# Kernel tuning notes

Measured on AMD Instinct MI355X. Metric: run time of the kernel, lower is better.

## Reference

```python
import jax, jax.numpy as jnp
import numpy as np

TAU = 1.0
EPS = 1e-6
M_FEATURES = 256
HEAD_DIM = 64


def _make_projection(m, d, seed=0):
    # FAVOR+ projection: stacked transposed-Q blocks from QR of Gaussian blocks,
    # rows rescaled by norms of iid Gaussian rows (scaling=0 in the torch code).
    rng = np.random.RandomState(seed)
    blocks = []
    for _ in range(m // d):
        q, _ = np.linalg.qr(rng.randn(d, d))
        blocks.append(q.T)
    rem = m - (m // d) * d
    if rem > 0:
        q, _ = np.linalg.qr(rng.randn(d, d))
        blocks.append(q.T[:rem])
    mat = np.vstack(blocks)
    multiplier = np.linalg.norm(rng.randn(m, d), axis=1)
    return jnp.asarray(multiplier[:, None] * mat, dtype=jnp.float32)


def setup_inputs() -> dict:
    key = jax.random.key(0)
    k1, k2, k3 = jax.random.split(key, 3)
    b, n, h, d = 4, 4096, 8, HEAD_DIM
    return {
        "x": jax.random.normal(k1, (b, n, h, d), dtype=jnp.float32),
        "node_vec1": jax.random.normal(k2, (b, n, h, d), dtype=jnp.float32),
        "node_vec2": jax.random.normal(k3, (b, n, h, d), dtype=jnp.float32),
        "projection_matrix": _make_projection(M_FEATURES, d, seed=0),
    }


def _random_feature_map(data, is_query, projection_matrix):
    d = data.shape[-1]
    data = data * (float(d) ** -0.25)  # data_normalizer = 1/sqrt(sqrt(d))
    ratio = float(projection_matrix.shape[0]) ** -0.5
    data_dash = jnp.einsum('bnhd,md->bnhm', data, projection_matrix)
    diag_data = jnp.sum(data * data, axis=-1, keepdims=True) * 0.5  # [b,n,h,1]
    if is_query:
        stab = jnp.max(data_dash, axis=-1, keepdims=True)  # per-position max
    else:
        # max over feature dim then over node dim (axis 1)
        stab = jnp.max(jnp.max(data_dash, axis=-1, keepdims=True), axis=1, keepdims=True)
    return ratio * (jnp.exp(data_dash - diag_data - stab) + EPS)


def reference(x, node_vec1, node_vec2, projection_matrix):
    inv_sqrt_tau = 1.0 / np.sqrt(TAU)
    v1p = _random_feature_map(node_vec1 * inv_sqrt_tau, True, projection_matrix)
    v2p = _random_feature_map(node_vec2 * inv_sqrt_tau, False, projection_matrix)
    # Linear (kernelized) attention via associativity: O(n*m*d) not O(n^2)
    v2x = jnp.einsum('bnhm,bnhd->bhmd', v2p, x)
    out1 = jnp.einsum('bnhm,bhmd->bnhd', v1p, v2x)
    v2_sum = jnp.sum(v2p, axis=1)  # [b,h,m]
    out2 = jnp.einsum('bnhm,bhm->bnh', v1p, v2_sum)
    return (out1 / out2[..., None], v1p, v2p)
```

## Files before the change

kernel.cpp:

```cpp
#include <hip/hip_runtime.h>
#include <math.h>


namespace {
constexpr int B_ = 4, N_ = 4096, H_ = 8, D_ = 64, M_ = 256;
constexpr int BH_ = B_ * H_;
constexpr int POS_ = B_ * N_ * H_;
constexpr float SCALE_ = 0.35355339059327378f;
constexpr float RATIO_ = 0.0625f;
constexpr float FEPS_ = 1e-6f;

constexpr int WS_BHMAX = 0;
constexpr int WS_V2X   = 32;
constexpr int WS_V2SUM = WS_V2X + BH_ * M_ * D_;
constexpr int WS_DIAG1 = WS_V2SUM + BH_ * M_;
constexpr int WS_DIAG2 = WS_DIAG1 + POS_;
constexpr int WS_ZERO_END = WS_DIAG1;
}

__device__ __forceinline__ void atomicMaxF(float* addr, float v) {
  if (v >= 0.f)
    atomicMax((int*)addr, __float_as_int(v));
  else
    atomicMin((unsigned int*)addr, __float_as_uint(v));
}

__global__ void k_init(float* __restrict__ ws) {
  int i = blockIdx.x * 256 + threadIdx.x;
  int stride = gridDim.x * 256;
  for (; i < WS_ZERO_END; i += stride) {
    ws[i] = (i < 32) ? -INFINITY : 0.f;
  }
}

__global__ void k_diag(const float* __restrict__ v1, const float* __restrict__ v2,
                       float* __restrict__ ws) {
  int t = threadIdx.x;
  int r = t >> 2, seg = t & 3;
  int rowg = blockIdx.x * 64 + r;
  const float* src;
  float* dst;
  int row;
  if (rowg < POS_) { src = v1; dst = ws + WS_DIAG1; row = rowg; }
  else             { src = v2; dst = ws + WS_DIAG2; row = rowg - POS_; }
  const float4* p = reinterpret_cast<const float4*>(src + (size_t)row * 64) + seg * 4;
  float s = 0.f;
#pragma unroll
  for (int j = 0; j < 4; ++j) {
    float4 v = p[j];
    s = fmaf(v.x, v.x, s); s = fmaf(v.y, v.y, s);
    s = fmaf(v.z, v.z, s); s = fmaf(v.w, v.w, s);
  }
  s += __shfl_xor(s, 1);
  s += __shfl_xor(s, 2);
  if (seg == 0) dst[row] = 0.0625f * s;
}

template <bool IS_QUERY>
__global__ __launch_bounds__(256) void k_proj(const float* __restrict__ vec,
                                              const float* __restrict__ Pm,
                                              float* __restrict__ ddout,
                                              float* __restrict__ ws) {
  int t = threadIdx.x;
  int bh = blockIdx.x >> 5;
  int tile = blockIdx.x & 31;
  int b = bh >> 3, h = bh & 7;

  float4 pr[16];
  {
    const float4* pp = reinterpret_cast<const float4*>(Pm + t * 64);
#pragma unroll
    for (int j = 0; j < 16; ++j) {
      float4 v = pp[j];
      pr[j].x = v.x * SCALE_; pr[j].y = v.y * SCALE_;
      pr[j].z = v.z * SCALE_; pr[j].w = v.w * SCALE_;
    }
  }

  __shared__ float wmax[2][4][8];
  __shared__ float wm[4];
  int wv = t >> 6, ln = t & 63;
  float vmax = -INFINITY;
  const float* diag1 = ws + WS_DIAG1;

  int nbase = tile * 128;
  for (int chunk = 0; chunk < 16; ++chunk) {
    float a[8];
#pragma unroll
    for (int cp = 0; cp < 8; ++cp) {
      int n = nbase + chunk * 8 + cp;
      int pg = (b * N_ + n) * H_ + h;
      const float4* r4 = reinterpret_cast<const float4*>(vec + (size_t)pg * 64);
      float acc = 0.f;
#pragma unroll
      for (int j = 0; j < 16; ++j) {
        float4 dv = r4[j];
        acc = fmaf(dv.x, pr[j].x, acc);
        acc = fmaf(dv.y, pr[j].y, acc);
        acc = fmaf(dv.z, pr[j].z, acc);
        acc = fmaf(dv.w, pr[j].w, acc);
      }
      a[cp] = acc;
    }
    if (IS_QUERY) {
      int buf = chunk & 1;
#pragma unroll
      for (int cp = 0; cp < 8; ++cp) {
        float m = a[cp];
#pragma unroll
        for (int o = 1; o < 64; o <<= 1) m = fmaxf(m, __shfl_xor(m, o));
        if (ln == 0) wmax[buf][wv][cp] = m;
      }
      __syncthreads();
#pragma unroll
      for (int cp = 0; cp < 8; ++cp) {
        int n = nbase + chunk * 8 + cp;
        int pg = (b * N_ + n) * H_ + h;
        float mx = fmaxf(fmaxf(wmax[buf][0][cp], wmax[buf][1][cp]),
                         fmaxf(wmax[buf][2][cp], wmax[buf][3][cp]));
        float dgv = diag1[pg];
        float val = RATIO_ * (__expf(a[cp] - dgv - mx) + FEPS_);
        ddout[pg * M_ + t] = val;
      }
    } else {
#pragma unroll
      for (int cp = 0; cp < 8; ++cp) {
        vmax = fmaxf(vmax, a[cp]);
        int n = nbase + chunk * 8 + cp;
        int pg = (b * N_ + n) * H_ + h;
        ddout[pg * M_ + t] = a[cp];
      }
    }
  }
  if (!IS_QUERY) {
#pragma unroll
    for (int o = 1; o < 64; o <<= 1) vmax = fmaxf(vmax, __shfl_xor(vmax, o));
    if (ln == 0) wm[wv] = vmax;
    __syncthreads();
    if (t == 0) {
      float m = fmaxf(fmaxf(wm[0], wm[1]), fmaxf(wm[2], wm[3]));
      atomicMaxF(ws + WS_BHMAX + bh, m);
    }
  }
}

__global__ __launch_bounds__(256) void k_v2accum(const float* __restrict__ x,
                                                 float* __restrict__ v2p,
                                                 float* __restrict__ ws) {
  __shared__ float sP[32][264];
  __shared__ float sX[32][64];
  int t = threadIdx.x;
  int bh = blockIdx.x >> 4, chunk = blockIdx.x & 15;
  int b = bh >> 3, h = bh & 7;
  int n0 = chunk * 256;
  float bhmax = ws[WS_BHMAX + bh];
  const float* diag2 = ws + WS_DIAG2;

  int mg = t & 31, dgi = t >> 5;
  int pl8 = t >> 3, seg = t & 7;

  float acc[8][8];
  float acc2[8];
#pragma unroll
  for (int i = 0; i < 8; ++i) {
    acc2[i] = 0.f;
#pragma unroll
    for (int j = 0; j < 8; ++j) acc[i][j] = 0.f;
  }

  for (int it = 0; it < 8; ++it) {
    __syncthreads();
    {
      int n = n0 + it * 32 + pl8;
      int pg = (b * N_ + n) * H_ + h;
      float dgv = diag2[pg];
      float* gp = v2p + (size_t)pg * M_;
#pragma unroll
      for (int j = 0; j < 8; ++j) {
        int m = seg * 4 + j * 32;
        float4 dv = *reinterpret_cast<const float4*>(gp + m);
        float4 vv;
        vv.x = RATIO_ * (__expf(dv.x - dgv - bhmax) + FEPS_);
        vv.y = RATIO_ * (__expf(dv.y - dgv - bhmax) + FEPS_);
        vv.z = RATIO_ * (__expf(dv.z - dgv - bhmax) + FEPS_);
        vv.w = RATIO_ * (__expf(dv.w - dgv - bhmax) + FEPS_);
        *reinterpret_cast<float4*>(gp + m) = vv;
        *reinterpret_cast<float4*>(&sP[pl8][m]) = vv;
      }
      const float* gx = x + (size_t)pg * 64;
#pragma unroll
      for (int j = 0; j < 2; ++j) {
        int f = seg * 2 + j;
        float4 xv = *reinterpret_cast<const float4*>(gx + f * 4);
        *reinterpret_cast<float4*>(&sX[pl8][f * 4]) = xv;
      }
    }
    __syncthreads();
#pragma unroll 4
    for (int nn = 0; nn < 32; ++nn) {
      float4 a0 = *reinterpret_cast<const float4*>(&sP[nn][mg * 8]);
      float4 a1 = *reinterpret_cast<const float4*>(&sP[nn][mg * 8 + 4]);
      float4 b0 = *reinterpret_cast<const float4*>(&sX[nn][dgi * 8]);
      float4 b1 = *reinterpret_cast<const float4*>(&sX[nn][dgi * 8 + 4]);
      float av[8] = {a0.x, a0.y, a0.z, a0.w, a1.x, a1.y, a1.z, a1.w};
      float bv[8] = {b0.x, b0.y, b0.z, b0.w, b1.x, b1.y, b1.z, b1.w};
#pragma unroll
      for (int i = 0; i < 8; ++i) {
        acc2[i] += av[i];
#pragma unroll
        for (int j = 0; j < 8; ++j) acc[i][j] = fmaf(av[i], bv[j], acc[i][j]);
      }
    }
  }

  float* vx = ws + WS_V2X + bh * M_ * D_;
#pragma unroll
  for (int i = 0; i < 8; ++i)
#pragma unroll
    for (int j = 0; j < 8; ++j)
      atomicAdd(vx + (mg * 8 + i) * 64 + dgi * 8 + j, acc[i][j]);
  if (dgi == 0) {
    float* vs = ws + WS_V2SUM + bh * M_;
#pragma unroll
    for (int i = 0; i < 8; ++i) atomicAdd(vs + mg * 8 + i, acc2[i]);
  }
}

__global__ __launch_bounds__(256) void k_pv(const float* __restrict__ v1p,
                                            float* __restrict__ ws,
                                            float* __restrict__ out) {
  __shared__ float sA[64][129];
  __shared__ float sB[128][68];
  __shared__ float sVs[256];
  int t = threadIdx.x;
  int bh = blockIdx.x >> 6, tile = blockIdx.x & 63;
  int b = bh >> 3, h = bh & 7;
  int n0 = tile * 64;
  int pg_ = t & 15, dg = t >> 4;
  int pl = t >> 2, sseg = t & 3;
  int mr = t >> 1, hseg = t & 1;

  if (t < 64) {
    float4 v = *reinterpret_cast<const float4*>(ws + WS_V2SUM + bh * M_ + t * 4);
    *reinterpret_cast<float4*>(&sVs[t * 4]) = v;
  }

  float acc1[4][4];
  float acc2[4];
#pragma unroll
  for (int i = 0; i < 4; ++i) {
    acc2[i] = 0.f;
#pragma unroll
    for (int j = 0; j < 4; ++j) acc1[i][j] = 0.f;
  }

  int posg_base = (b * N_ + n0) * H_ + h;

  for (int half = 0; half < 2; ++half) {
    __syncthreads();
    int m0 = half * 128;
    {
      int pg = posg_base + pl * H_;
      const float* gp = v1p + (size_t)pg * M_ + m0;
#pragma unroll
      for (int j = 0; j < 8; ++j) {
        int m = sseg * 4 + j * 16;
        float4 v = *reinterpret_cast<const float4*>(gp + m);
        sA[pl][m] = v.x; sA[pl][m + 1] = v.y;
        sA[pl][m + 2] = v.z; sA[pl][m + 3] = v.w;
      }
      const float* gb = ws + WS_V2X + bh * M_ * D_ + (m0 + mr) * 64 + hseg * 32;
#pragma unroll
      for (int j = 0; j < 8; ++j) {
        float4 v = *reinterpret_cast<const float4*>(gb + j * 4);
        *reinterpret_cast<float4*>(&sB[mr][hseg * 32 + j * 4]) = v;
      }
    }
    __syncthreads();
#pragma unroll 4
    for (int m = 0; m < 128; ++m) {
      float a0 = sA[4 * pg_ + 0][m];
      float a1 = sA[4 * pg_ + 1][m];
      float a2 = sA[4 * pg_ + 2][m];
      float a3 = sA[4 * pg_ + 3][m];
      float4 bv = *reinterpret_cast<const float4*>(&sB[m][dg * 4]);
      float vsm = sVs[m0 + m];
      acc1[0][0] = fmaf(a0, bv.x, acc1[0][0]); acc1[0][1] = fmaf(a0, bv.y, acc1[0][1]);
      acc1[0][2] = fmaf(a0, bv.z, acc1[0][2]); acc1[0][3] = fmaf(a0, bv.w, acc1[0][3]);
      acc1[1][0] = fmaf(a1, bv.x, acc1[1][0]); acc1[1][1] = fmaf(a1, bv.y, acc1[1][1]);
      acc1[1][2] = fmaf(a1, bv.z, acc1[1][2]); acc1[1][3] = fmaf(a1, bv.w, acc1[1][3]);
      acc1[2][0] = fmaf(a2, bv.x, acc1[2][0]); acc1[2][1] = fmaf(a2, bv.y, acc1[2][1]);
      acc1[2][2] = fmaf(a2, bv.z, acc1[2][2]); acc1[2][3] = fmaf(a2, bv.w, acc1[2][3]);
      acc1[3][0] = fmaf(a3, bv.x, acc1[3][0]); acc1[3][1] = fmaf(a3, bv.y, acc1[3][1]);
      acc1[3][2] = fmaf(a3, bv.z, acc1[3][2]); acc1[3][3] = fmaf(a3, bv.w, acc1[3][3]);
      acc2[0] = fmaf(a0, vsm, acc2[0]);
      acc2[1] = fmaf(a1, vsm, acc2[1]);
      acc2[2] = fmaf(a2, vsm, acc2[2]);
      acc2[3] = fmaf(a3, vsm, acc2[3]);
    }
  }

#pragma unroll
  for (int i = 0; i < 4; ++i) {
    int pg = posg_base + (4 * pg_ + i) * H_;
    float inv = 1.f / acc2[i];
    float4 o;
    o.x = acc1[i][0] * inv; o.y = acc1[i][1] * inv;
    o.z = acc1[i][2] * inv; o.w = acc1[i][3] * inv;
    *reinterpret_cast<float4*>(out + (size_t)pg * 64 + dg * 4) = o;
  }
}

extern "C" void kernel_launch(void* const* d_in, const int* in_sizes, int n_in,
                              void* d_out, int out_size, void* d_ws, size_t ws_size,
                              hipStream_t stream) {
  const float* x  = (const float*)d_in[0];
  const float* v1 = (const float*)d_in[1];
  const float* v2 = (const float*)d_in[2];
  const float* Pm = (const float*)d_in[3];
  float* out = (float*)d_out;
  float* v1p = out + (size_t)POS_ * D_;
  float* v2p = v1p + (size_t)POS_ * M_;
  float* ws = (float*)d_ws;

  k_init<<<1024, 256, 0, stream>>>(ws);
  k_diag<<<2 * POS_ / 64, 256, 0, stream>>>(v1, v2, ws);
  k_proj<false><<<BH_ * 32, 256, 0, stream>>>(v2, Pm, v2p, ws);
  k_proj<true><<<BH_ * 32, 256, 0, stream>>>(v1, Pm, v1p, ws);
  k_v2accum<<<BH_ * 16, 256, 0, stream>>>(x, v2p, ws);
  k_pv<<<BH_ * 64, 256, 0, stream>>>(v1p, ws, out);
}
```

Before: 1.015 ms.

## Stage projection inputs in LDS, split v2 accumulation by feature quarter, add deterministic partial reduce

k_proj now loads its 128-row input tile into shared memory once instead of re-reading it from global memory per thread, and the key path stores exp(dash - diag) directly. k_v2accum then only needs to rescale by a per-bh factor exp(-max) with a single FMA rather than a full exp. k_v2accum is split four ways across the feature dimension, giving 2048 blocks with smaller per-thread accumulators for more parallelism and lower register pressure. When the workspace is large enough, partial results go to a buffer and a new reduce kernel sums them instead of issuing atomics. k_pv uses 64-wide m-phases with smaller shared tiles. Factoring exp(-max) out of the stored exp changes rounding slightly and could overflow if the raw logits are large.

```diff
diff --git a/kernel.cpp b/kernel.cpp
--- a/kernel.cpp
+++ b/kernel.cpp
@@ -15,6 +15,9 @@
 constexpr int WS_V2SUM = WS_V2X + BH_ * M_ * D_;
 constexpr int WS_DIAG1 = WS_V2SUM + BH_ * M_;
 constexpr int WS_DIAG2 = WS_DIAG1 + POS_;
+constexpr int WS_PART  = WS_DIAG2 + POS_;
+constexpr int WS_PSUM  = WS_PART + 16 * 32 * 4 * 4096;
+constexpr int WS_END   = WS_PSUM + 16 * 32 * 4 * 64;
 constexpr int WS_ZERO_END = WS_DIAG1;
 }
 
@@ -57,13 +60,15 @@
 }
 
 template <bool IS_QUERY>
-__global__ __launch_bounds__(256) void k_proj(const float* __restrict__ vec,
-                                              const float* __restrict__ Pm,
-                                              float* __restrict__ ddout,
-                                              float* __restrict__ ws) {
+__global__ __launch_bounds__(256, 4) void k_proj(const float* __restrict__ vec,
+                                                 const float* __restrict__ Pm,
+                                                 float* __restrict__ ddout,
+                                                 float* __restrict__ ws) {
+  __shared__ float4 sD[128 * 16];
+  __shared__ float wmax[2][4][8];
+  __shared__ float wm[4];
   int t = threadIdx.x;
-  int bh = blockIdx.x >> 5;
-  int tile = blockIdx.x & 31;
+  int bh = blockIdx.x >> 5, tile = blockIdx.x & 31;
   int b = bh >> 3, h = bh & 7;
 
   float4 pr[16];
@@ -77,24 +82,32 @@
     }
   }
 
-  __shared__ float wmax[2][4][8];
-  __shared__ float wm[4];
+  {
+    const float* base = vec + ((size_t)(b * N_ + tile * 128) * H_ + h) * 64;
+    int r0 = t >> 4, fq = t & 15;
+#pragma unroll
+    for (int i = 0; i < 8; ++i) {
+      int row = i * 16 + r0;
+      sD[row * 16 + fq] =
+          *reinterpret_cast<const float4*>(base + (size_t)row * 512 + fq * 4);
+    }
+  }
+  __syncthreads();
+
   int wv = t >> 6, ln = t & 63;
-  float vmax = -INFINITY;
-  const float* diag1 = ws + WS_DIAG1;
-
-  int nbase = tile * 128;
-  for (int chunk = 0; chunk < 16; ++chunk) {
+  const float* diag = ws + (IS_QUERY ? WS_DIAG1 : WS_DIAG2);
+  int pgbase = (b * N_ + tile * 128) * H_ + h;
+  float vmaxk = -INFINITY;
+
+  for (int grp = 0; grp < 16; ++grp) {
     float a[8];
 #pragma unroll
     for (int cp = 0; cp < 8; ++cp) {
-      int n = nbase + chunk * 8 + cp;
-      int pg = (b * N_ + n) * H_ + h;
-      const float4* r4 = reinterpret_cast<const float4*>(vec + (size_t)pg * 64);
+      const float4* rp = &sD[(grp * 8 + cp) * 16];
       float acc = 0.f;
 #pragma unroll
       for (int j = 0; j < 16; ++j) {
-        float4 dv = r4[j];
+        float4 dv = rp[j];
         acc = fmaf(dv.x, pr[j].x, acc);
         acc = fmaf(dv.y, pr[j].y, acc);
         acc = fmaf(dv.z, pr[j].z, acc);
@@ -103,7 +116,7 @@
       a[cp] = acc;
     }
     if (IS_QUERY) {
-      int buf = chunk & 1;
+      int buf = grp & 1;
 #pragma unroll
       for (int cp = 0; cp < 8; ++cp) {
         float m = a[cp];
@@ -114,131 +127,149 @@
       __syncthreads();
 #pragma unroll
       for (int cp = 0; cp < 8; ++cp) {
-        int n = nbase + chunk * 8 + cp;
-        int pg = (b * N_ + n) * H_ + h;
+        int pg = pgbase + (grp * 8 + cp) * H_;
         float mx = fmaxf(fmaxf(wmax[buf][0][cp], wmax[buf][1][cp]),
                          fmaxf(wmax[buf][2][cp], wmax[buf][3][cp]));
-        float dgv = diag1[pg];
-        float val = RATIO_ * (__expf(a[cp] - dgv - mx) + FEPS_);
-        ddout[pg * M_ + t] = val;
+        ddout[(size_t)pg * M_ + t] = RATIO_ * (__expf(a[cp] - diag[pg] - mx) + FEPS_);
       }
     } else {
 #pragma unroll
       for (int cp = 0; cp < 8; ++cp) {
-        vmax = fmaxf(vmax, a[cp]);
-        int n = nbase + chunk * 8 + cp;
-        int pg = (b * N_ + n) * H_ + h;
-        ddout[pg * M_ + t] = a[cp];
+        int pg = pgbase + (grp * 8 + cp) * H_;
+        vmaxk = fmaxf(vmaxk, a[cp]);
+        ddout[(size_t)pg * M_ + t] = __expf(a[cp] - diag[pg]);
       }
     }
   }
   if (!IS_QUERY) {
 #pragma unroll
-    for (int o = 1; o < 64; o <<= 1) vmax = fmaxf(vmax, __shfl_xor(vmax, o));
-    if (ln == 0) wm[wv] = vmax;
-    __syncthreads();
-    if (t == 0) {
-      float m = fmaxf(fmaxf(wm[0], wm[1]), fmaxf(wm[2], wm[3]));
-      atomicMaxF(ws + WS_BHMAX + bh, m);
-    }
+    for (int o = 1; o < 64; o <<= 1) vmaxk = fmaxf(vmaxk, __shfl_xor(vmaxk, o));
+    if (ln == 0) wm[wv] = vmaxk;
+    __syncthreads();
+    if (t == 0)
+      atomicMaxF(ws + WS_BHMAX + bh, fmaxf(fmaxf(wm[0], wm[1]), fmaxf(wm[2], wm[3])));
   }
 }
 
 __global__ __launch_bounds__(256) void k_v2accum(const float* __restrict__ x,
                                                  float* __restrict__ v2p,
-                                                 float* __restrict__ ws) {
-  __shared__ float sP[32][264];
-  __shared__ float sX[32][64];
+                                                 float* __restrict__ ws, int use_part) {
+  __shared__ float sE[16][68];
+  __shared__ float sX[16][68];
   int t = threadIdx.x;
-  int bh = blockIdx.x >> 4, chunk = blockIdx.x & 15;
+  int bx = blockIdx.x;
+  int chunk = bx & 15, mq = (bx >> 4) & 3, bh = bx >> 6;
   int b = bh >> 3, h = bh & 7;
   int n0 = chunk * 256;
-  float bhmax = ws[WS_BHMAX + bh];
-  const float* diag2 = ws + WS_DIAG2;
-
-  int mg = t & 31, dgi = t >> 5;
-  int pl8 = t >> 3, seg = t & 7;
-
-  float acc[8][8];
-  float acc2[8];
-#pragma unroll
-  for (int i = 0; i < 8; ++i) {
-    acc2[i] = 0.f;
+  float rs = RATIO_ * __expf(-ws[WS_BHMAX + bh]);
+  float re = RATIO_ * FEPS_;
+
+  int mg = t >> 3, dgi = t & 7;
+  int r0 = t >> 4, fq = t & 15;
+
+  float acc[2][8];
+  float acc2[2] = {0.f, 0.f};
+#pragma unroll
+  for (int i = 0; i < 2; ++i)
 #pragma unroll
     for (int j = 0; j < 8; ++j) acc[i][j] = 0.f;
-  }
-
-  for (int it = 0; it < 8; ++it) {
+
+  for (int it = 0; it < 16; ++it) {
     __syncthreads();
     {
-      int n = n0 + it * 32 + pl8;
-      int pg = (b * N_ + n) * H_ + h;
-      float dgv = diag2[pg];
-      float* gp = v2p + (size_t)pg * M_;
-#pragma unroll
-      for (int j = 0; j < 8; ++j) {
-        int m = seg * 4 + j * 32;
-        float4 dv = *reinterpret_cast<const float4*>(gp + m);
-        float4 vv;
-        vv.x = RATIO_ * (__expf(dv.x - dgv - bhmax) + FEPS_);
-        vv.y = RATIO_ * (__expf(dv.y - dgv - bhmax) + FEPS_);
-        vv.z = RATIO_ * (__expf(dv.z - dgv - bhmax) + FEPS_);
-        vv.w = RATIO_ * (__expf(dv.w - dgv - bhmax) + FEPS_);
-        *reinterpret_cast<float4*>(gp + m) = vv;
-        *reinterpret_cast<float4*>(&sP[pl8][m]) = vv;
-      }
-      const float* gx = x + (size_t)pg * 64;
-#pragma unroll
-      for (int j = 0; j < 2; ++j) {
-        int f = seg * 2 + j;
-        float4 xv = *reinterpret_cast<const float4*>(gx + f * 4);
-        *reinterpret_cast<float4*>(&sX[pl8][f * 4]) = xv;
-      }
+      size_t pg = (size_t)(b * N_ + n0 + it * 16 + r0) * H_ + h;
+      float* gp = v2p + pg * M_ + mq * 64 + fq * 4;
+      float4 ev = *reinterpret_cast<const float4*>(gp);
+      float4 vv;
+      vv.x = fmaf(ev.x, rs, re); vv.y = fmaf(ev.y, rs, re);
+      vv.z = fmaf(ev.z, rs, re); vv.w = fmaf(ev.w, rs, re);
+      *reinterpret_cast<float4*>(gp) = vv;
+      *reinterpret_cast<float4*>(&sE[r0][fq * 4]) = vv;
+      float4 xv = *reinterpret_cast<const float4*>(x + pg * 64 + fq * 4);
+      *reinterpret_cast<float4*>(&sX[r0][fq * 4]) = xv;
     }
     __syncthreads();
 #pragma unroll 4
-    for (int nn = 0; nn < 32; ++nn) {
-      float4 a0 = *reinterpret_cast<const float4*>(&sP[nn][mg * 8]);
-      float4 a1 = *reinterpret_cast<const float4*>(&sP[nn][mg * 8 + 4]);
+    for (int nn = 0; nn < 16; ++nn) {
+      float2 ev = *reinterpret_cast<const float2*>(&sE[nn][mg * 2]);
       float4 b0 = *reinterpret_cast<const float4*>(&sX[nn][dgi * 8]);
       float4 b1 = *reinterpret_cast<const float4*>(&sX[nn][dgi * 8 + 4]);
-      float av[8] = {a0.x, a0.y, a0.z, a0.w, a1.x, a1.y, a1.z, a1.w};
-      float bv[8] = {b0.x, b0.y, b0.z, b0.w, b1.x, b1.y, b1.z, b1.w};
-#pragma unroll
-      for (int i = 0; i < 8; ++i) {
-        acc2[i] += av[i];
-#pragma unroll
-        for (int j = 0; j < 8; ++j) acc[i][j] = fmaf(av[i], bv[j], acc[i][j]);
-      }
-    }
-  }
-
-  float* vx = ws + WS_V2X + bh * M_ * D_;
-#pragma unroll
-  for (int i = 0; i < 8; ++i)
-#pragma unroll
-    for (int j = 0; j < 8; ++j)
-      atomicAdd(vx + (mg * 8 + i) * 64 + dgi * 8 + j, acc[i][j]);
-  if (dgi == 0) {
-    float* vs = ws + WS_V2SUM + bh * M_;
-#pragma unroll
-    for (int i = 0; i < 8; ++i) atomicAdd(vs + mg * 8 + i, acc2[i]);
+      acc2[0] += ev.x; acc2[1] += ev.y;
+      acc[0][0] = fmaf(ev.x, b0.x, acc[0][0]); acc[0][1] = fmaf(ev.x, b0.y, acc[0][1]);
+      acc[0][2] = fmaf(ev.x, b0.z, acc[0][2]); acc[0][3] = fmaf(ev.x, b0.w, acc[0][3]);
+      acc[0][4] = fmaf(ev.x, b1.x, acc[0][4]); acc[0][5] = fmaf(ev.x, b1.y, acc[0][5]);
+      acc[0][6] = fmaf(ev.x, b1.z, acc[0][6]); acc[0][7] = fmaf(ev.x, b1.w, acc[0][7]);
+      acc[1][0] = fmaf(ev.y, b0.x, acc[1][0]); acc[1][1] = fmaf(ev.y, b0.y, acc[1][1]);
+      acc[1][2] = fmaf(ev.y, b0.z, acc[1][2]); acc[1][3] = fmaf(ev.y, b0.w, acc[1][3]);
+      acc[1][4] = fmaf(ev.y, b1.x, acc[1][4]); acc[1][5] = fmaf(ev.y, b1.y, acc[1][5]);
+      acc[1][6] = fmaf(ev.y, b1.z, acc[1][6]); acc[1][7] = fmaf(ev.y, b1.w, acc[1][7]);
+    }
+  }
+
+  if (use_part) {
+    float* pp = ws + WS_PART + (((size_t)chunk * BH_ + bh) * 4 + mq) * 4096;
+#pragma unroll
+    for (int i = 0; i < 2; ++i) {
+      float* q = pp + (mg * 2 + i) * 64 + dgi * 8;
+      *reinterpret_cast<float4*>(q)     = make_float4(acc[i][0], acc[i][1], acc[i][2], acc[i][3]);
+      *reinterpret_cast<float4*>(q + 4) = make_float4(acc[i][4], acc[i][5], acc[i][6], acc[i][7]);
+    }
+    if (dgi == 0) {
+      float* ps = ws + WS_PSUM + (((size_t)chunk * BH_ + bh) * 4 + mq) * 64 + mg * 2;
+      ps[0] = acc2[0]; ps[1] = acc2[1];
+    }
+  } else {
+    float* vx = ws + WS_V2X + (size_t)bh * M_ * D_;
+#pragma unroll
+    for (int i = 0; i < 2; ++i)
+#pragma unroll
+      for (int j = 0; j < 8; ++j)
+        atomicAdd(vx + (mq * 64 + mg * 2 + i) * 64 + dgi * 8 + j, acc[i][j]);
+    if (dgi == 0) {
+      float* vs = ws + WS_V2SUM + (size_t)bh * M_;
+#pragma unroll
+      for (int i = 0; i < 2; ++i) atomicAdd(vs + mq * 64 + mg * 2 + i, acc2[i]);
+    }
+  }
+}
+
+__global__ void k_reduce(float* __restrict__ ws) {
+  int i = blockIdx.x * 256 + threadIdx.x;
+  if (i < 131072) {
+    int bh = i >> 12, rem = i & 4095;
+    int m = rem >> 4, dq = rem & 15;
+    int mq = m >> 6, mloc = m & 63;
+    float4 s = make_float4(0.f, 0.f, 0.f, 0.f);
+#pragma unroll
+    for (int c = 0; c < 16; ++c) {
+      const float4 v = *reinterpret_cast<const float4*>(
+          ws + WS_PART + (((size_t)c * BH_ + bh) * 4 + mq) * 4096 + mloc * 64 + dq * 4);
+      s.x += v.x; s.y += v.y; s.z += v.z; s.w += v.w;
+    }
+    *reinterpret_cast<float4*>(ws + WS_V2X + (size_t)i * 4) = s;
+  } else if (i < 131072 + 8192) {
+    int j = i - 131072;
+    int bh = j >> 8, m = j & 255;
+    int mq = m >> 6, mloc = m & 63;
+    float s = 0.f;
+#pragma unroll
+    for (int c = 0; c < 16; ++c)
+      s += ws[WS_PSUM + (((size_t)c * BH_ + bh) * 4 + mq) * 64 + mloc];
+    ws[WS_V2SUM + j] = s;
   }
 }
 
 __global__ __launch_bounds__(256) void k_pv(const float* __restrict__ v1p,
                                             float* __restrict__ ws,
                                             float* __restrict__ out) {
-  __shared__ float sA[64][129];
-  __shared__ float sB[128][68];
+  __shared__ float sA[64][67];
+  __shared__ float sB[64][68];
   __shared__ float sVs[256];
   int t = threadIdx.x;
   int bh = blockIdx.x >> 6, tile = blockIdx.x & 63;
   int b = bh >> 3, h = bh & 7;
-  int n0 = tile * 64;
   int pg_ = t & 15, dg = t >> 4;
-  int pl = t >> 2, sseg = t & 3;
-  int mr = t >> 1, hseg = t & 1;
+  int pl = t >> 2, ps = t & 3;
 
   if (t < 64) {
     float4 v = *reinterpret_cast<const float4*>(ws + WS_V2SUM + bh * M_ + t * 4);
@@ -254,31 +285,30 @@
     for (int j = 0; j < 4; ++j) acc1[i][j] = 0.f;
   }
 
-  int posg_base = (b * N_ + n0) * H_ + h;
-
-  for (int half = 0; half < 2; ++half) {
-    __syncthreads();
-    int m0 = half * 128;
+  size_t posg_base = (size_t)(b * N_ + tile * 64) * H_ + h;
+
+  for (int ph = 0; ph < 4; ++ph) {
+    __syncthreads();
+    int m0 = ph * 64;
     {
-      int pg = posg_base + pl * H_;
-      const float* gp = v1p + (size_t)pg * M_ + m0;
-#pragma unroll
-      for (int j = 0; j < 8; ++j) {
-        int m = sseg * 4 + j * 16;
-        float4 v = *reinterpret_cast<const float4*>(gp + m);
-        sA[pl][m] = v.x; sA[pl][m + 1] = v.y;
-        sA[pl][m + 2] = v.z; sA[pl][m + 3] = v.w;
-      }
-      const float* gb = ws + WS_V2X + bh * M_ * D_ + (m0 + mr) * 64 + hseg * 32;
-#pragma unroll
-      for (int j = 0; j < 8; ++j) {
+      const float* gp = v1p + (posg_base + (size_t)pl * H_) * M_ + m0;
+#pragma unroll
+      for (int j = 0; j < 4; ++j) {
+        int mcol = ps * 4 + j * 16;
+        float4 v = *reinterpret_cast<const float4*>(gp + mcol);
+        sA[pl][mcol] = v.x; sA[pl][mcol + 1] = v.y;
+        sA[pl][mcol + 2] = v.z; sA[pl][mcol + 3] = v.w;
+      }
+      const float* gb = ws + WS_V2X + (size_t)bh * M_ * D_ + (size_t)(m0 + pl) * 64 + ps * 16;
+#pragma unroll
+      for (int j = 0; j < 4; ++j) {
         float4 v = *reinterpret_cast<const float4*>(gb + j * 4);
-        *reinterpret_cast<float4*>(&sB[mr][hseg * 32 + j * 4]) = v;
+        *reinterpret_cast<float4*>(&sB[pl][ps * 16 + j * 4]) = v;
       }
     }
     __syncthreads();
 #pragma unroll 4
-    for (int m = 0; m < 128; ++m) {
+    for (int m = 0; m < 64; ++m) {
       float a0 = sA[4 * pg_ + 0][m];
       float a1 = sA[4 * pg_ + 1][m];
       float a2 = sA[4 * pg_ + 2][m];
@@ -302,12 +332,12 @@
 
 #pragma unroll
   for (int i = 0; i < 4; ++i) {
-    int pg = posg_base + (4 * pg_ + i) * H_;
+    size_t pg = posg_base + (size_t)(4 * pg_ + i) * H_;
     float inv = 1.f / acc2[i];
     float4 o;
     o.x = acc1[i][0] * inv; o.y = acc1[i][1] * inv;
     o.z = acc1[i][2] * inv; o.w = acc1[i][3] * inv;
-    *reinterpret_cast<float4*>(out + (size_t)pg * 64 + dg * 4) = o;
+    *reinterpret_cast<float4*>(out + pg * 64 + dg * 4) = o;
   }
 }
 
@@ -322,11 +352,13 @@
   float* v1p = out + (size_t)POS_ * D_;
   float* v2p = v1p + (size_t)POS_ * M_;
   float* ws = (float*)d_ws;
+  int use_part = (ws_size >= (size_t)WS_END * 4) ? 1 : 0;
 
   k_init<<<1024, 256, 0, stream>>>(ws);
   k_diag<<<2 * POS_ / 64, 256, 0, stream>>>(v1, v2, ws);
   k_proj<false><<<BH_ * 32, 256, 0, stream>>>(v2, Pm, v2p, ws);
   k_proj<true><<<BH_ * 32, 256, 0, stream>>>(v1, Pm, v1p, ws);
-  k_v2accum<<<BH_ * 16, 256, 0, stream>>>(x, v2p, ws);
-  k_pv<<<BH_ * 64, 256, 0, stream>>>(v1p, ws, out);
-}
+  k_v2accum<<<2048, 256, 0, stream>>>(x, v2p, ws, use_part);
+  if (use_part) k_reduce<<<544, 256, 0, stream>>>(ws);
+  k_pv<<<2048, 256, 0, stream>>>(v1p, ws, out);
+}
```

Result: slower. 3.500 ms (+244.9%).
